# Performance work log

Measured on AMD Instinct MI355X. Metric: run time of the kernel, lower is better.

Reference implementation:

```python
import jax, jax.numpy as jnp
import numpy as np

N = 50000      # nodes
E = 800000     # edges (before self loops)
IN = 128       # input feature dim
HID = 64       # hidden channels per head
H = 4          # heads
OUT = 1        # final out channels
D1 = H * HID   # 256, concat feature dim
NEG_SLOPE = 0.2


def _p(k, shape):
    return jax.random.normal(k, shape, jnp.float32) * 0.1


def setup_inputs() -> dict:
    key = jax.random.key(0)
    ks = jax.random.split(key, 32)
    inp = {
        "x": jax.random.normal(ks[0], (N, IN), jnp.float32),
        "edge_index": jax.random.randint(ks[1], (2, E), 0, N, dtype=jnp.int32),
        "batch": jnp.zeros((N,), jnp.int32),
    }
    # layer 0: GATConv(IN -> HID, heads=H, concat) ; Linear(IN -> H*HID)
    inp["cW0"] = _p(ks[2], (IN, H * HID)); inp["cas0"] = _p(ks[3], (H, HID))
    inp["cad0"] = _p(ks[4], (H, HID));     inp["cb0"] = jnp.zeros((D1,), jnp.float32)
    inp["lW0"] = _p(ks[5], (IN, D1));      inp["lb0"] = jnp.zeros((D1,), jnp.float32)
    # layer 1: GATConv(D1 -> HID, heads=H, concat) ; Linear(D1 -> D1)
    inp["cW1"] = _p(ks[6], (D1, H * HID)); inp["cas1"] = _p(ks[7], (H, HID))
    inp["cad1"] = _p(ks[8], (H, HID));     inp["cb1"] = jnp.zeros((D1,), jnp.float32)
    inp["lW1"] = _p(ks[9], (D1, D1));      inp["lb1"] = jnp.zeros((D1,), jnp.float32)
    # layer 2: GATConv(D1 -> OUT, heads=H, concat=False -> mean) ; Linear(D1 -> OUT)
    inp["cW2"] = _p(ks[10], (D1, H * OUT)); inp["cas2"] = _p(ks[11], (H, OUT))
    inp["cad2"] = _p(ks[12], (H, OUT));     inp["cb2"] = jnp.zeros((OUT,), jnp.float32)
    inp["lW2"] = _p(ks[13], (D1, OUT));     inp["lb2"] = jnp.zeros((OUT,), jnp.float32)
    return inp


def gat_conv(x, W, att_src, att_dst, bias, src, dst, out_c, concat):
    """PyG-style GATConv with self loops already included in (src, dst)."""
    n = x.shape[0]
    xl = (x @ W).reshape(n, H, out_c)                  # [N,H,C]
    a_s = (xl * att_src).sum(-1)                       # [N,H]
    a_d = (xl * att_dst).sum(-1)                       # [N,H]
    e = jax.nn.leaky_relu(a_s[src] + a_d[dst], NEG_SLOPE)   # [Et,H]
    # numerically stable segment softmax over destination nodes
    e_max = jax.ops.segment_max(e, dst, num_segments=n)
    ex = jnp.exp(e - e_max[dst])
    denom = jax.ops.segment_sum(ex, dst, num_segments=n)
    alpha = ex / (denom[dst] + 1e-16)                  # [Et,H]
    msg = xl[src] * alpha[..., None]                   # [Et,H,C]
    out = jax.ops.segment_sum(msg, dst, num_segments=n)  # [N,H,C]
    out = out.reshape(n, H * out_c) if concat else out.mean(axis=1)
    return out + bias


def _forward(x, edge_index,
             cW0, cas0, cad0, cb0, lW0, lb0,
             cW1, cas1, cad1, cb1, lW1, lb1,
             cW2, cas2, cad2, cb2, lW2, lb2):
    n = x.shape[0]
    loop = jnp.arange(n, dtype=edge_index.dtype)
    src = jnp.concatenate([edge_index[0], loop])
    dst = jnp.concatenate([edge_index[1], loop])
    h = jax.nn.elu(gat_conv(x, cW0, cas0, cad0, cb0, src, dst, HID, True) + (x @ lW0 + lb0))
    h = jax.nn.elu(gat_conv(h, cW1, cas1, cad1, cb1, src, dst, HID, True) + (h @ lW1 + lb1))
    return gat_conv(h, cW2, cas2, cad2, cb2, src, dst, OUT, False) + (h @ lW2 + lb2)


def reference(x, edge_index, batch,
              cW0, cas0, cad0, cb0, lW0, lb0,
              cW1, cas1, cad1, cb1, lW1, lb1,
              cW2, cas2, cad2, cb2, lW2, lb2):
    return _forward(x, edge_index,
                    cW0, cas0, cad0, cb0, lW0, lb0,
                    cW1, cas1, cad1, cb1, lW1, lb1,
                    cW2, cas2, cad2, cb2, lW2, lb2)
```

## Files before the change

### kernel.cpp

```cpp
#include <hip/hip_runtime.h>
#include <cstddef>
#include <cstdint>

#define NN 50000
#define EE 800000
#define ET_ (EE + NN)

typedef __attribute__((ext_vector_type(8))) short bf16x8;
typedef __attribute__((ext_vector_type(4))) float f32x4;

__device__ __forceinline__ float lrelu_(float x) { return x > 0.f ? x : 0.2f * x; }
__device__ __forceinline__ float elu_(float x)   { return x > 0.f ? x : (__expf(x) - 1.f); }
__device__ __forceinline__ short f2bf(float f) {
    unsigned u = __float_as_uint(f);
    unsigned r = (u + 0x7fffu + ((u >> 16) & 1u)) >> 16;
    return (short)r;
}
__device__ __forceinline__ float bflo(unsigned u) { return __uint_as_float(u << 16); }
__device__ __forceinline__ float bfhi(unsigned u) { return __uint_as_float(u & 0xffff0000u); }

#define GL16(gp, lp) __builtin_amdgcn_global_load_lds( \
    (const __attribute__((address_space(1))) unsigned int*)(gp), \
    (__attribute__((address_space(3))) unsigned int*)(lp), 16, 0, 0)


__global__ __launch_bounds__(256) void prep_all(const float* __restrict__ x,
                                                const float* __restrict__ cW0, const float* __restrict__ lW0,
                                                const float* __restrict__ cW1, const float* __restrict__ lW1,
                                                const int* __restrict__ ei, int* __restrict__ deg,
                                                short* __restrict__ xb, short* __restrict__ Wt0,
                                                short* __restrict__ Wt1) {
    int i = blockIdx.x * 256 + threadIdx.x;
    if (i < 1600000) {
        float4 v = *(const float4*)(x + (size_t)i * 4);
        short4 o;
        o.x = f2bf(v.x); o.y = f2bf(v.y); o.z = f2bf(v.z); o.w = f2bf(v.w);
        *(short4*)(xb + (size_t)i * 4) = o;
        return;
    }
    i -= 1600000;
    if (i < 512 * 128) {
        int n = i >> 7, k = i & 127;
        float v = (n < 256) ? cW0[k * 256 + n] : lW0[k * 256 + (n - 256)];
        Wt0[i] = f2bf(v);
        return;
    }
    i -= 512 * 128;
    if (i < 512 * 256) {
        int n = i >> 8, k = i & 255;
        float v = (n < 256) ? cW1[k * 256 + n] : lW1[k * 256 + (n - 256)];
        Wt1[i] = f2bf(v);
        return;
    }
    i -= 512 * 256;
    if (i < ET_) {
        int d = (i < EE) ? ei[EE + i] : (i - EE);
        atomicAdd(&deg[d], 1);
    }
}


__global__ __launch_bounds__(1024) void alloc_scan(const int* __restrict__ deg, int* __restrict__ rowptr,
                                                   int* __restrict__ gcnt, int n) {
    __shared__ int s[1024];
    __shared__ int basesh;
    int tid = threadIdx.x;
    int gid = blockIdx.x * 1024 + tid;
    int v = (gid < n) ? deg[gid] : 0;
    s[tid] = v;
    __syncthreads();
    for (int off = 1; off < 1024; off <<= 1) {
        int t = (tid >= off) ? s[tid - off] : 0;
        __syncthreads();
        s[tid] += t;
        __syncthreads();
    }
    if (tid == 1023) basesh = atomicAdd(gcnt, s[1023]);
    __syncthreads();
    if (gid < n) rowptr[gid] = basesh + s[tid] - v;
}

__global__ __launch_bounds__(256) void scatter_k(const int* __restrict__ ei,
                                                 const int* __restrict__ rowptr,
                                                 int* __restrict__ cursor,
                                                 int* __restrict__ csr_src) {
    int e = blockIdx.x * blockDim.x + threadIdx.x;
    if (e >= ET_) return;
    int s, d;
    if (e < EE) { s = ei[e]; d = ei[EE + e]; } else { s = e - EE; d = e - EE; }
    int pos = atomicAdd(&cursor[d], 1);
    csr_src[rowptr[d] + pos] = s;
}


__global__ __launch_bounds__(256) void gemm_bf16(const short* __restrict__ A,
                                                 const short* __restrict__ Wt,
                                                 const float* __restrict__ biasLin,
                                                 short* __restrict__ XLb,
                                                 short* __restrict__ Hlinb,
                                                 int M, int K) {
    __shared__ short smem[4][128 * 32];
    const int tid = threadIdx.x;
    const int lane = tid & 63;
    const int wid = tid >> 6;
    const int bm = blockIdx.x * 128;
    const int col0 = blockIdx.y * 128;
    const int wr = wid >> 1, wc = wid & 1;

    f32x4 acc[4][4];
#pragma unroll
    for (int i = 0; i < 4; ++i)
#pragma unroll
        for (int j = 0; j < 4; ++j) acc[i][j] = (f32x4){0.f, 0.f, 0.f, 0.f};

    const int lrow = lane & 15, lk = lane >> 4;

    auto stage = [&](int b, int kk) {
#pragma unroll
        for (int it = 0; it < 2; ++it) {
            const int flat = tid + it * 256;
            const int row = flat >> 2, slot = flat & 3;
            const int ss = slot ^ (row & 3);
            int ar = bm + row; ar = (ar < M) ? ar : (M - 1);
            GL16(A + (size_t)ar * K + kk + ss * 8, &smem[b][flat * 8]);
            GL16(Wt + (size_t)(col0 + row) * K + kk + ss * 8, &smem[2 + b][flat * 8]);
        }
    };

    stage(0, 0);
    int cur = 0;
    for (int k0 = 0; k0 < K; k0 += 32) {
        __syncthreads();
        if (k0 + 32 < K) stage(cur ^ 1, k0 + 32);
        bf16x8 af[4], bfr[4];
#pragma unroll
        for (int mi = 0; mi < 4; ++mi) {
            const int r = wr * 64 + mi * 16 + lrow;
            af[mi] = *(const bf16x8*)(&smem[cur][(r * 4 + (lk ^ (r & 3))) * 8]);
        }
#pragma unroll
        for (int ni = 0; ni < 4; ++ni) {
            const int c = wc * 64 + ni * 16 + lrow;
            bfr[ni] = *(const bf16x8*)(&smem[2 + cur][(c * 4 + (lk ^ (c & 3))) * 8]);
        }
#pragma unroll
        for (int mi = 0; mi < 4; ++mi)
#pragma unroll
            for (int ni = 0; ni < 4; ++ni)
                acc[mi][ni] = __builtin_amdgcn_mfma_f32_16x16x32_bf16(af[mi], bfr[ni], acc[mi][ni], 0, 0, 0);
        cur ^= 1;
    }

    __syncthreads();
    short* Ct = &smem[0][0];
    const bool isLin = (col0 >= 256);
    float bni[4] = {0.f, 0.f, 0.f, 0.f};
    if (isLin) {
#pragma unroll
        for (int ni = 0; ni < 4; ++ni)
            bni[ni] = biasLin[col0 - 256 + wc * 64 + ni * 16 + lrow];
    }
    const int lrow4 = lk * 4;
#pragma unroll
    for (int mi = 0; mi < 4; ++mi) {
#pragma unroll
        for (int ni = 0; ni < 4; ++ni) {
            const int col_l = wc * 64 + ni * 16 + lrow;
#pragma unroll
            for (int rr = 0; rr < 4; ++rr) {
                const int row_l = wr * 64 + mi * 16 + lrow4 + rr;
                const int idx = (row_l * 128 + col_l) ^ (((row_l >> 2) & 3) << 4);
                Ct[idx] = f2bf(acc[mi][ni][rr] + bni[ni]);
            }
        }
    }
    __syncthreads();

    short* outp = isLin ? Hlinb : XLb;
    const int gcol0 = isLin ? (col0 - 256) : col0;
#pragma unroll
    for (int rr8 = 0; rr8 < 8; ++rr8) {
        const int flat = tid + rr8 * 256;
        const int row = flat >> 4, seg = flat & 15;
        const int sidx = (row * 128 + seg * 8) ^ (((row >> 2) & 3) << 4);
        if (bm + row < M) {
            bf16x8 vv = *(const bf16x8*)(Ct + sidx);
            *(bf16x8*)(outp + (size_t)(bm + row) * 256 + gcol0 + seg * 8) = vv;
        }
    }
}


__global__ __launch_bounds__(256) void attn_prep(const short* __restrict__ XLb,
                                                 const float* __restrict__ cas,
                                                 const float* __restrict__ cad,
                                                 float* __restrict__ AS,
                                                 float* __restrict__ AD, int n_nodes) {
    int n = (blockIdx.x * blockDim.x + threadIdx.x) >> 6;
    int lane = threadIdx.x & 63;
    if (n >= n_nodes) return;
    uint2 q = *(const uint2*)(XLb + (size_t)n * 256 + lane * 4);
    float x0 = bflo(q.x), x1 = bfhi(q.x);
    float x2 = bflo(q.y), x3 = bfhi(q.y);
    float4 sv = *(const float4*)(cas + lane * 4);
    float4 dv = *(const float4*)(cad + lane * 4);
    float ps = x0 * sv.x + x1 * sv.y + x2 * sv.z + x3 * sv.w;
    float pd = x0 * dv.x + x1 * dv.y + x2 * dv.z + x3 * dv.w;
#pragma unroll
    for (int off = 1; off < 16; off <<= 1) {
        ps += __shfl_xor(ps, off);
        pd += __shfl_xor(pd, off);
    }
    if ((lane & 15) == 0) {
        AS[n * 4 + (lane >> 4)] = ps;
        AD[n * 4 + (lane >> 4)] = pd;
    }
}


__global__ __launch_bounds__(256) void gat_agg(const short* __restrict__ XLb,
                                               const float* __restrict__ AS,
                                               const float* __restrict__ AD,
                                               const int* __restrict__ rowptr,
                                               const int* __restrict__ degarr,
                                               const int* __restrict__ csr_src,
                                               const float* __restrict__ cb,
                                               const short* __restrict__ Hlinb,
                                               short* __restrict__ Hb,
                                               const float* __restrict__ cW2,
                                               const float* __restrict__ lW2,
                                               const float* __restrict__ lb2,
                                               float* __restrict__ XL2,
                                               float* __restrict__ LIN2,
                                               int n_nodes) {
    __shared__ int   sIdx[4][64];
    __shared__ float sExT[4][4][72];

    const int tid = threadIdx.x;
    const int lane = tid & 63;
    const int w = tid >> 6;
    const int n = blockIdx.x * 4 + w;
    if (n >= n_nodes) return;

    const int rs = rowptr[n];
    const int deg = degarr[n];
    const float4 ad4 = *(const float4*)(AD + n * 4);

    const int half = lane >> 5;
    const int l32 = lane & 31;
    const int ch0 = l32 * 8;
    const int h = l32 >> 3;

    float4 acc0 = make_float4(0.f, 0.f, 0.f, 0.f);
    float4 acc1 = make_float4(0.f, 0.f, 0.f, 0.f);
    float d0 = 0.f, d1 = 0.f, d2 = 0.f, d3 = 0.f;

    auto ACC = [&](const uint4& q, float e) {
        acc0.x += e * bflo(q.x); acc0.y += e * bfhi(q.x);
        acc0.z += e * bflo(q.y); acc0.w += e * bfhi(q.y);
        acc1.x += e * bflo(q.z); acc1.y += e * bfhi(q.z);
        acc1.z += e * bflo(q.w); acc1.w += e * bfhi(q.w);
    };

    if (deg <= 64) {
        int sv = 0;
        float c0 = -1e30f, c1 = -1e30f, c2 = -1e30f, c3 = -1e30f;
        if (lane < deg) {
            sv = csr_src[rs + lane];
            float4 a = *(const float4*)(AS + sv * 4);
            c0 = lrelu_(a.x + ad4.x); c1 = lrelu_(a.y + ad4.y);
            c2 = lrelu_(a.z + ad4.z); c3 = lrelu_(a.w + ad4.w);
        }
        float m0 = c0, m1 = c1, m2 = c2, m3 = c3;
#pragma unroll
        for (int off = 32; off > 0; off >>= 1) {
            m0 = fmaxf(m0, __shfl_xor(m0, off));
            m1 = fmaxf(m1, __shfl_xor(m1, off));
            m2 = fmaxf(m2, __shfl_xor(m2, off));
            m3 = fmaxf(m3, __shfl_xor(m3, off));
        }
        float e0 = 0.f, e1 = 0.f, e2 = 0.f, e3 = 0.f;
        if (lane < deg) {
            e0 = __expf(c0 - m0); e1 = __expf(c1 - m1);
            e2 = __expf(c2 - m2); e3 = __expf(c3 - m3);
        }
        sIdx[w][lane] = sv;
        sExT[w][0][lane] = e0; sExT[w][1][lane] = e1;
        sExT[w][2][lane] = e2; sExT[w][3][lane] = e3;
        d0 = e0; d1 = e1; d2 = e2; d3 = e3;
        __builtin_amdgcn_wave_barrier();

        const int cpad = (deg + 1) & ~1;
        int j = 0;
        for (; j + 8 <= cpad; j += 8) {
            int ja = j + half, jb = j + 2 + half, jc = j + 4 + half, jd = j + 6 + half;
            int sa = sIdx[w][ja], sb = sIdx[w][jb], sc = sIdx[w][jc], sd = sIdx[w][jd];
            float ea = sExT[w][h][ja], eb = sExT[w][h][jb];
            float ec = sExT[w][h][jc], ed = sExT[w][h][jd];
            uint4 qa = *(const uint4*)(XLb + (size_t)sa * 256 + ch0);
            uint4 qb = *(const uint4*)(XLb + (size_t)sb * 256 + ch0);
            uint4 qc = *(const uint4*)(XLb + (size_t)sc * 256 + ch0);
            uint4 qd = *(const uint4*)(XLb + (size_t)sd * 256 + ch0);
            ACC(qa, ea); ACC(qb, eb); ACC(qc, ec); ACC(qd, ed);
        }
        for (; j < cpad; j += 2) {
            int jj = j + half;
            int s = sIdx[w][jj];
            float e = sExT[w][h][jj];
            uint4 q = *(const uint4*)(XLb + (size_t)s * 256 + ch0);
            ACC(q, e);
        }
    } else {
        float m0 = -1e30f, m1 = -1e30f, m2 = -1e30f, m3 = -1e30f;
        for (int base = 0; base < deg; base += 64) {
            int idx = base + lane;
            if (idx < deg) {
                int s = csr_src[rs + idx];
                float4 a = *(const float4*)(AS + s * 4);
                m0 = fmaxf(m0, lrelu_(a.x + ad4.x));
                m1 = fmaxf(m1, lrelu_(a.y + ad4.y));
                m2 = fmaxf(m2, lrelu_(a.z + ad4.z));
                m3 = fmaxf(m3, lrelu_(a.w + ad4.w));
            }
        }
#pragma unroll
        for (int off = 32; off > 0; off >>= 1) {
            m0 = fmaxf(m0, __shfl_xor(m0, off));
            m1 = fmaxf(m1, __shfl_xor(m1, off));
            m2 = fmaxf(m2, __shfl_xor(m2, off));
            m3 = fmaxf(m3, __shfl_xor(m3, off));
        }
        for (int base = 0; base < deg; base += 64) {
            int cnt = deg - base; if (cnt > 64) cnt = 64;
            int idx = base + lane;
            int sv = 0;
            float e0 = 0.f, e1 = 0.f, e2 = 0.f, e3 = 0.f;
            if (idx < deg) {
                sv = csr_src[rs + idx];
                float4 a = *(const float4*)(AS + sv * 4);
                e0 = __expf(lrelu_(a.x + ad4.x) - m0);
                e1 = __expf(lrelu_(a.y + ad4.y) - m1);
                e2 = __expf(lrelu_(a.z + ad4.z) - m2);
                e3 = __expf(lrelu_(a.w + ad4.w) - m3);
            }
            sIdx[w][lane] = sv;
            sExT[w][0][lane] = e0; sExT[w][1][lane] = e1;
            sExT[w][2][lane] = e2; sExT[w][3][lane] = e3;
            d0 += e0; d1 += e1; d2 += e2; d3 += e3;
            __builtin_amdgcn_wave_barrier();
            int cpad = (cnt + 1) & ~1;
            for (int j = 0; j < cpad; j += 2) {
                int jj = j + half;
                int s = sIdx[w][jj];
                float e = sExT[w][h][jj];
                uint4 q = *(const uint4*)(XLb + (size_t)s * 256 + ch0);
                ACC(q, e);
            }
            __builtin_amdgcn_wave_barrier();
        }
    }

    acc0.x += __shfl_xor(acc0.x, 32); acc0.y += __shfl_xor(acc0.y, 32);
    acc0.z += __shfl_xor(acc0.z, 32); acc0.w += __shfl_xor(acc0.w, 32);
    acc1.x += __shfl_xor(acc1.x, 32); acc1.y += __shfl_xor(acc1.y, 32);
    acc1.z += __shfl_xor(acc1.z, 32); acc1.w += __shfl_xor(acc1.w, 32);
#pragma unroll
    for (int off = 32; off > 0; off >>= 1) {
        d0 += __shfl_xor(d0, off); d1 += __shfl_xor(d1, off);
        d2 += __shfl_xor(d2, off); d3 += __shfl_xor(d3, off);
    }
    float den = (h == 0) ? d0 : (h == 1) ? d1 : (h == 2) ? d2 : d3;
    float inv = 1.f / (den + 1e-16f);

    float v0 = 0.f, v1 = 0.f, v2 = 0.f, v3 = 0.f, v4 = 0.f, v5 = 0.f, v6 = 0.f, v7 = 0.f;
    if (lane < 32) {
        size_t o = (size_t)n * 256 + ch0;
        uint4 hq = *(const uint4*)(Hlinb + o);
        float4 cba = *(const float4*)(cb + ch0);
        float4 cbb = *(const float4*)(cb + ch0 + 4);
        v0 = elu_(acc0.x * inv + cba.x + bflo(hq.x));
        v1 = elu_(acc0.y * inv + cba.y + bfhi(hq.x));
        v2 = elu_(acc0.z * inv + cba.z + bflo(hq.y));
        v3 = elu_(acc0.w * inv + cba.w + bfhi(hq.y));
        v4 = elu_(acc1.x * inv + cbb.x + bflo(hq.z));
        v5 = elu_(acc1.y * inv + cbb.y + bfhi(hq.z));
        v6 = elu_(acc1.z * inv + cbb.z + bflo(hq.w));
        v7 = elu_(acc1.w * inv + cbb.w + bfhi(hq.w));
    }

    if (XL2 != nullptr) {
        float p0 = 0.f, p1 = 0.f, p2 = 0.f, p3 = 0.f, pl = 0.f;
        if (lane < 32) {
            const float vv[8] = {v0, v1, v2, v3, v4, v5, v6, v7};
            float4 lwa = *(const float4*)(lW2 + ch0);
            float4 lwb = *(const float4*)(lW2 + ch0 + 4);
            const float lw[8] = {lwa.x, lwa.y, lwa.z, lwa.w, lwb.x, lwb.y, lwb.z, lwb.w};
#pragma unroll
            for (int j = 0; j < 8; ++j) {
                float4 wv = *(const float4*)(cW2 + (ch0 + j) * 4);
                p0 += vv[j] * wv.x; p1 += vv[j] * wv.y;
                p2 += vv[j] * wv.z; p3 += vv[j] * wv.w;
                pl += vv[j] * lw[j];
            }
        }
#pragma unroll
        for (int off = 16; off > 0; off >>= 1) {
            p0 += __shfl_xor(p0, off); p1 += __shfl_xor(p1, off);
            p2 += __shfl_xor(p2, off); p3 += __shfl_xor(p3, off);
            pl += __shfl_xor(pl, off);
        }
        if (lane == 0) {
            *(float4*)(XL2 + n * 4) = make_float4(p0, p1, p2, p3);
            LIN2[n] = pl + lb2[0];
        }
    } else if (lane < 32) {
        size_t o = (size_t)n * 256 + ch0;
        uint4 ov;
        ov.x = (unsigned)(unsigned short)f2bf(v0) | ((unsigned)(unsigned short)f2bf(v1) << 16);
        ov.y = (unsigned)(unsigned short)f2bf(v2) | ((unsigned)(unsigned short)f2bf(v3) << 16);
        ov.z = (unsigned)(unsigned short)f2bf(v4) | ((unsigned)(unsigned short)f2bf(v5) << 16);
        ov.w = (unsigned)(unsigned short)f2bf(v6) | ((unsigned)(unsigned short)f2bf(v7) << 16);
        *(uint4*)(Hb + o) = ov;
    }
}


__global__ __launch_bounds__(256) void l2_agg(const float* __restrict__ XL2,
                                              const float* __restrict__ LIN2,
                                              const float* __restrict__ cas2,
                                              const float* __restrict__ cad2,
                                              const float* __restrict__ cb2,
                                              const int* __restrict__ rowptr,
                                              const int* __restrict__ degarr,
                                              const int* __restrict__ csr_src,
                                              float* __restrict__ out, int n_nodes) {
    int n = (blockIdx.x * blockDim.x + threadIdx.x) >> 6;
    int lane = threadIdx.x & 63;
    if (n >= n_nodes) return;
    int rs = rowptr[n], re = rs + degarr[n];
    float4 xn = *(const float4*)(XL2 + n * 4);
    float cs0 = cas2[0], cs1 = cas2[1], cs2 = cas2[2], cs3 = cas2[3];
    float cd0 = cad2[0], cd1 = cad2[1], cd2 = cad2[2], cd3 = cad2[3];
    float ad0 = xn.x * cd0, ad1 = xn.y * cd1, ad2 = xn.z * cd2, ad3 = xn.w * cd3;

    float m0 = -1e30f, m1 = -1e30f, m2 = -1e30f, m3 = -1e30f;
    for (int i = rs + lane; i < re; i += 64) {
        int s = csr_src[i];
        float4 xs = *(const float4*)(XL2 + s * 4);
        m0 = fmaxf(m0, lrelu_(xs.x * cs0 + ad0));
        m1 = fmaxf(m1, lrelu_(xs.y * cs1 + ad1));
        m2 = fmaxf(m2, lrelu_(xs.z * cs2 + ad2));
        m3 = fmaxf(m3, lrelu_(xs.w * cs3 + ad3));
    }
#pragma unroll
    for (int off = 32; off > 0; off >>= 1) {
        m0 = fmaxf(m0, __shfl_xor(m0, off));
        m1 = fmaxf(m1, __shfl_xor(m1, off));
        m2 = fmaxf(m2, __shfl_xor(m2, off));
        m3 = fmaxf(m3, __shfl_xor(m3, off));
    }

    float d0 = 0.f, d1 = 0.f, d2 = 0.f, d3 = 0.f;
    float t0 = 0.f, t1 = 0.f, t2 = 0.f, t3 = 0.f;
    for (int i = rs + lane; i < re; i += 64) {
        int s = csr_src[i];
        float4 xs = *(const float4*)(XL2 + s * 4);
        float e0 = __expf(lrelu_(xs.x * cs0 + ad0) - m0);
        float e1 = __expf(lrelu_(xs.y * cs1 + ad1) - m1);
        float e2 = __expf(lrelu_(xs.z * cs2 + ad2) - m2);
        float e3 = __expf(lrelu_(xs.w * cs3 + ad3) - m3);
        d0 += e0; d1 += e1; d2 += e2; d3 += e3;
        t0 += e0 * xs.x; t1 += e1 * xs.y; t2 += e2 * xs.z; t3 += e3 * xs.w;
    }
#pragma unroll
    for (int off = 32; off > 0; off >>= 1) {
        d0 += __shfl_xor(d0, off); d1 += __shfl_xor(d1, off);
        d2 += __shfl_xor(d2, off); d3 += __shfl_xor(d3, off);
        t0 += __shfl_xor(t0, off); t1 += __shfl_xor(t1, off);
        t2 += __shfl_xor(t2, off); t3 += __shfl_xor(t3, off);
    }
    if (lane == 0) {
        float r = 0.25f * (t0 / (d0 + 1e-16f) + t1 / (d1 + 1e-16f) +
                           t2 / (d2 + 1e-16f) + t3 / (d3 + 1e-16f));
        out[n] = r + cb2[0] + LIN2[n];
    }
}


extern "C" void kernel_launch(void* const* d_in, const int* in_sizes, int n_in,
                              void* d_out, int out_size, void* d_ws, size_t ws_size,
                              hipStream_t stream) {
    const float* x    = (const float*)d_in[0];
    const int*   ei   = (const int*)d_in[1];
    const float* cW0  = (const float*)d_in[3];
    const float* cas0 = (const float*)d_in[4];
    const float* cad0 = (const float*)d_in[5];
    const float* cb0  = (const float*)d_in[6];
    const float* lW0  = (const float*)d_in[7];
    const float* lb0  = (const float*)d_in[8];
    const float* cW1  = (const float*)d_in[9];
    const float* cas1 = (const float*)d_in[10];
    const float* cad1 = (const float*)d_in[11];
    const float* cb1  = (const float*)d_in[12];
    const float* lW1  = (const float*)d_in[13];
    const float* lb1  = (const float*)d_in[14];
    const float* cW2  = (const float*)d_in[15];
    const float* cas2 = (const float*)d_in[16];
    const float* cad2 = (const float*)d_in[17];
    const float* cb2  = (const float*)d_in[18];
    const float* lW2  = (const float*)d_in[19];
    const float* lb2  = (const float*)d_in[20];
    float* out = (float*)d_out;

    short* xb    = (short*)d_ws;
    short* XLb   = xb + 6400000;
    short* HAb   = XLb + 12800000;
    short* Hlinb = HAb + 12800000;
    short* Wt0   = Hlinb + 12800000;
    short* Wt1   = Wt0 + 65536;
    float* AS    = (float*)(Wt1 + 131072);
    float* AD    = AS + 200000;
    float* XL2   = AD + 200000;
    float* LIN2  = XL2 + 200000;
    int* deg     = (int*)(LIN2 + NN);
    int* cursor  = deg + NN;
    int* gcnt    = cursor + NN;
    int* rowptr  = gcnt + 4;
    int* csr_src = rowptr + NN;

    dim3 b256(256);
    dim3 gEdges((ET_ + 255) / 256);
    dim3 gNodesWave((NN + 3) / 4);

    hipMemsetAsync(deg, 0, (2 * (size_t)NN + 4) * sizeof(int), stream);
    prep_all<<<dim3(10339), b256, 0, stream>>>(x, cW0, lW0, cW1, lW1, ei, deg, xb, Wt0, Wt1);
    alloc_scan<<<dim3((NN + 1023) / 1024), dim3(1024), 0, stream>>>(deg, rowptr, gcnt, NN);
    scatter_k<<<gEdges, b256, 0, stream>>>(ei, rowptr, cursor, csr_src);

    dim3 gemmGrid((NN + 127) / 128, 4);

    gemm_bf16<<<gemmGrid, b256, 0, stream>>>(xb, Wt0, lb0, XLb, Hlinb, NN, 128);
    attn_prep<<<gNodesWave, b256, 0, stream>>>(XLb, cas0, cad0, AS, AD, NN);
    gat_agg<<<gNodesWave, b256, 0, stream>>>(XLb, AS, AD, rowptr, deg, csr_src, cb0, Hlinb,
                                             HAb, nullptr, nullptr, nullptr, nullptr, nullptr, NN);

    gemm_bf16<<<gemmGrid, b256, 0, stream>>>(HAb, Wt1, lb1, XLb, Hlinb, NN, 256);
    attn_prep<<<gNodesWave, b256, 0, stream>>>(XLb, cas1, cad1, AS, AD, NN);
    gat_agg<<<gNodesWave, b256, 0, stream>>>(XLb, AS, AD, rowptr, deg, csr_src, cb1, Hlinb,
                                             nullptr, cW2, lW2, lb2, XL2, LIN2, NN);

    l2_agg<<<gNodesWave, b256, 0, stream>>>(XL2, LIN2, cas2, cad2, cb2, rowptr, deg, csr_src, out, NN);
}
```

Measured before the change: 462.2 us.

## Fuse attention-score projection into GEMM epilogue and deepen gather unroll

Removes the separate attn_prep kernel by computing the per-head source/destination attention dot products inside the GEMM epilogue, using the bf16 tile already held in shared memory with shuffle reductions over 8-lane groups. This saves two kernel launches and a full re-read of XLb per layer. The aggregation loop also gets a 16-edge unrolled stage that issues 8 independent row gathers before accumulating, for more memory-level parallelism, at the cost of extra register pressure.

New measurement: 466.7 us. Within noise of the previous version (+1.0%).

```diff
diff --git a/kernel.cpp b/kernel.cpp
--- a/kernel.cpp
+++ b/kernel.cpp
@@ -18,6 +18,7 @@
 }
 __device__ __forceinline__ float bflo(unsigned u) { return __uint_as_float(u << 16); }
 __device__ __forceinline__ float bfhi(unsigned u) { return __uint_as_float(u & 0xffff0000u); }
+__device__ __forceinline__ float bfs(short s) { return __uint_as_float(((unsigned)(unsigned short)s) << 16); }
 
 #define GL16(gp, lp) __builtin_amdgcn_global_load_lds( \
     (const __attribute__((address_space(1))) unsigned int*)(gp), \
@@ -96,8 +97,12 @@
 __global__ __launch_bounds__(256) void gemm_bf16(const short* __restrict__ A,
                                                  const short* __restrict__ Wt,
                                                  const float* __restrict__ biasLin,
+                                                 const float* __restrict__ attS,
+                                                 const float* __restrict__ attD,
                                                  short* __restrict__ XLb,
                                                  short* __restrict__ Hlinb,
+                                                 float* __restrict__ AS,
+                                                 float* __restrict__ AD,
                                                  int M, int K) {
     __shared__ short smem[4][128 * 32];
     const int tid = threadIdx.x;
@@ -178,42 +183,39 @@
 
     short* outp = isLin ? Hlinb : XLb;
     const int gcol0 = isLin ? (col0 - 256) : col0;
+    const int seg = tid & 15;
+    float4 sA0, sA1, sD0, sD1;
+    if (!isLin) {
+        sA0 = *(const float4*)(attS + col0 + seg * 8);
+        sA1 = *(const float4*)(attS + col0 + seg * 8 + 4);
+        sD0 = *(const float4*)(attD + col0 + seg * 8);
+        sD1 = *(const float4*)(attD + col0 + seg * 8 + 4);
+    }
 #pragma unroll
     for (int rr8 = 0; rr8 < 8; ++rr8) {
         const int flat = tid + rr8 * 256;
-        const int row = flat >> 4, seg = flat & 15;
+        const int row = flat >> 4;
         const int sidx = (row * 128 + seg * 8) ^ (((row >> 2) & 3) << 4);
-        if (bm + row < M) {
-            bf16x8 vv = *(const bf16x8*)(Ct + sidx);
-            *(bf16x8*)(outp + (size_t)(bm + row) * 256 + gcol0 + seg * 8) = vv;
-        }
-    }
-}
-
-
-__global__ __launch_bounds__(256) void attn_prep(const short* __restrict__ XLb,
-                                                 const float* __restrict__ cas,
-                                                 const float* __restrict__ cad,
-                                                 float* __restrict__ AS,
-                                                 float* __restrict__ AD, int n_nodes) {
-    int n = (blockIdx.x * blockDim.x + threadIdx.x) >> 6;
-    int lane = threadIdx.x & 63;
-    if (n >= n_nodes) return;
-    uint2 q = *(const uint2*)(XLb + (size_t)n * 256 + lane * 4);
-    float x0 = bflo(q.x), x1 = bfhi(q.x);
-    float x2 = bflo(q.y), x3 = bfhi(q.y);
-    float4 sv = *(const float4*)(cas + lane * 4);
-    float4 dv = *(const float4*)(cad + lane * 4);
-    float ps = x0 * sv.x + x1 * sv.y + x2 * sv.z + x3 * sv.w;
-    float pd = x0 * dv.x + x1 * dv.y + x2 * dv.z + x3 * dv.w;
-#pragma unroll
-    for (int off = 1; off < 16; off <<= 1) {
-        ps += __shfl_xor(ps, off);
-        pd += __shfl_xor(pd, off);
-    }
-    if ((lane & 15) == 0) {
-        AS[n * 4 + (lane >> 4)] = ps;
-        AD[n * 4 + (lane >> 4)] = pd;
+        const int grow = bm + row;
+        bf16x8 vv = *(const bf16x8*)(Ct + sidx);
+        if (grow < M)
+            *(bf16x8*)(outp + (size_t)grow * 256 + gcol0 + seg * 8) = vv;
+        if (!isLin) {
+            float f0 = bfs(vv[0]), f1 = bfs(vv[1]), f2 = bfs(vv[2]), f3 = bfs(vv[3]);
+            float f4 = bfs(vv[4]), f5 = bfs(vv[5]), f6 = bfs(vv[6]), f7 = bfs(vv[7]);
+            float sp = f0 * sA0.x + f1 * sA0.y + f2 * sA0.z + f3 * sA0.w
+                     + f4 * sA1.x + f5 * sA1.y + f6 * sA1.z + f7 * sA1.w;
+            float dp = f0 * sD0.x + f1 * sD0.y + f2 * sD0.z + f3 * sD0.w
+                     + f4 * sD1.x + f5 * sD1.y + f6 * sD1.z + f7 * sD1.w;
+            sp += __shfl_xor(sp, 1); dp += __shfl_xor(dp, 1);
+            sp += __shfl_xor(sp, 2); dp += __shfl_xor(dp, 2);
+            sp += __shfl_xor(sp, 4); dp += __shfl_xor(dp, 4);
+            if ((seg & 7) == 0 && grow < M) {
+                const int hh = (col0 >> 6) + (seg >> 3);
+                AS[grow * 4 + hh] = sp;
+                AD[grow * 4 + hh] = dp;
+            }
+        }
     }
 }
 
@@ -292,6 +294,15 @@
 
         const int cpad = (deg + 1) & ~1;
         int j = 0;
+        for (; j + 16 <= cpad; j += 16) {
+            int jj[8]; int ss[8]; float ee[8]; uint4 qq[8];
+#pragma unroll
+            for (int u = 0; u < 8; ++u) { jj[u] = j + 2 * u + half; ss[u] = sIdx[w][jj[u]]; ee[u] = sExT[w][h][jj[u]]; }
+#pragma unroll
+            for (int u = 0; u < 8; ++u) qq[u] = *(const uint4*)(XLb + (size_t)ss[u] * 256 + ch0);
+#pragma unroll
+            for (int u = 0; u < 8; ++u) ACC(qq[u], ee[u]);
+        }
         for (; j + 8 <= cpad; j += 8) {
             int ja = j + half, jb = j + 2 + half, jc = j + 4 + half, jd = j + 6 + half;
             int sa = sIdx[w][ja], sb = sIdx[w][jb], sc = sIdx[w][jc], sd = sIdx[w][jd];
@@ -539,13 +550,11 @@
 
     dim3 gemmGrid((NN + 127) / 128, 4);
 
-    gemm_bf16<<<gemmGrid, b256, 0, stream>>>(xb, Wt0, lb0, XLb, Hlinb, NN, 128);
-    attn_prep<<<gNodesWave, b256, 0, stream>>>(XLb, cas0, cad0, AS, AD, NN);
+    gemm_bf16<<<gemmGrid, b256, 0, stream>>>(xb, Wt0, lb0, cas0, cad0, XLb, Hlinb, AS, AD, NN, 128);
     gat_agg<<<gNodesWave, b256, 0, stream>>>(XLb, AS, AD, rowptr, deg, csr_src, cb0, Hlinb,
                                              HAb, nullptr, nullptr, nullptr, nullptr, nullptr, NN);
 
-    gemm_bf16<<<gemmGrid, b256, 0, stream>>>(HAb, Wt1, lb1, XLb, Hlinb, NN, 256);
-    attn_prep<<<gNodesWave, b256, 0, stream>>>(XLb, cas1, cad1, AS, AD, NN);
+    gemm_bf16<<<gemmGrid, b256, 0, stream>>>(HAb, Wt1, lb1, cas1, cad1, XLb, Hlinb, AS, AD, NN, 256);
     gat_agg<<<gNodesWave, b256, 0, stream>>>(XLb, AS, AD, rowptr, deg, csr_src, cb1, Hlinb,
                                              nullptr, cW2, lW2, lb2, XL2, LIN2, NN);
 
```
